# Kernel optimization log

Measured on AMD Instinct MI355X. Metric: run time of the kernel, lower is better.

The kernel has to match this reference:

```python
import jax, jax.numpy as jnp
import numpy as np

RF = 13          # receptive field with defaults
N_LAYERS = 8     # blocks(4) * layers(2)
DIMS = 32
RC = 16          # residual/dilation channels
SC = 8           # skip channels
BN_EPS = 1e-5


def conv1x1(x, W, b=None):
    # x: (B,Cin,N,T), W: (Cout,Cin)
    y = jnp.einsum('oc,bcnt->bont', W, x)
    if b is not None:
        y = y + b[None, :, None, None]
    return y


def bn_eval(x, g, b):
    # eval-mode BatchNorm2d with running_mean=0, running_var=1
    return x * (g / jnp.sqrt(1.0 + BN_EPS))[None, :, None, None] + b[None, :, None, None]


def setup_inputs() -> dict:
    key = jax.random.key(0)
    ks = jax.random.split(key, 24)
    B, N, T, days = 16, 1024, 12, 288
    inp = {}
    inp['inputs'] = jax.random.normal(ks[0], (B, 2, N, T), dtype=jnp.float32)
    inp['ind'] = jax.random.randint(ks[1], (B,), 0, days)
    # start convs (1 -> RC)
    inp['start_w'] = jax.random.normal(ks[2], (RC, 1)) * 0.05
    inp['start_b'] = jax.random.normal(ks[3], (RC,)) * 0.05
    inp['starta_w'] = jax.random.normal(ks[4], (RC, 1)) * 0.05
    inp['starta_b'] = jax.random.normal(ks[5], (RC,)) * 0.05
    # dynamic-graph node embeddings (torch.randn init)
    inp['p1'] = jax.random.normal(ks[6], (days, DIMS))
    inp['p2'] = jax.random.normal(ks[7], (N, DIMS))
    inp['p3'] = jax.random.normal(ks[8], (N, DIMS))
    inp['pk'] = jax.random.normal(ks[9], (DIMS, DIMS, DIMS))
    # shared channel-attention fcs (bias=False)
    inp['fc1_w'] = jax.random.normal(ks[10], (RC, RC)) * 0.05
    inp['fc2_w'] = jax.random.normal(ks[11], (RC, RC)) * 0.05
    # per-layer skip convs (RC -> SC)
    inp['skip_w'] = jax.random.normal(ks[12], (N_LAYERS, SC, RC)) * 0.05
    inp['skip_b'] = jax.random.normal(ks[13], (N_LAYERS, SC)) * 0.05
    # per-layer gcn mlp ((order*support_len+1)*RC = 48 -> RC)
    inp['gconv_w'] = jax.random.normal(ks[14], (N_LAYERS, RC, 3 * RC)) * 0.05
    inp['gconv_b'] = jax.random.normal(ks[15], (N_LAYERS, RC)) * 0.05
    # batchnorm affine params
    inp['bn_g'] = jnp.ones((N_LAYERS, RC)) + jax.random.normal(ks[16], (N_LAYERS, RC)) * 0.01
    inp['bn_b'] = jax.random.normal(ks[17], (N_LAYERS, RC)) * 0.01
    inp['bna_g'] = jnp.ones((N_LAYERS, RC)) + jax.random.normal(ks[18], (N_LAYERS, RC)) * 0.01
    inp['bna_b'] = jax.random.normal(ks[19], (N_LAYERS, RC)) * 0.01
    # end convs: 832 -> 64 -> 12
    inp['end1_w'] = jax.random.normal(ks[20], (64, SC * RF * N_LAYERS)) * 0.02
    inp['end1_b'] = jax.random.normal(ks[21], (64,)) * 0.02
    inp['end2_w'] = jax.random.normal(ks[22], (12, 64)) * 0.02
    inp['end2_b'] = jax.random.normal(ks[23], (12,)) * 0.02
    return inp


def reference(inputs, ind, start_w, start_b, starta_w, starta_b, p1, p2, p3, pk,
              fc1_w, fc2_w, skip_w, skip_b, gconv_w, gconv_b,
              bn_g, bn_b, bna_g, bna_b, end1_w, end1_b, end2_w, end2_b):
    B, _, N, T = inputs.shape
    if T < RF:  # static python condition
        xo = jnp.pad(inputs, ((0, 0), (0, 0), (0, 0), (RF - T, 0)))
    else:
        xo = inputs
    x = conv1x1(xo[:, 0:1], start_w, start_b)      # (B,RC,N,RF)
    x_a = conv1x1(xo[:, 1:2], starta_w, starta_b)  # (B,RC,N,RF)

    # dgconstruct: dynamic adjacency (identical for every layer -> compute once)
    te = p1[ind]                                   # (B,DIMS)
    adp = jnp.einsum('ai,ijk->ajk', te, pk)        # (B,DIMS,DIMS)
    src = jnp.einsum('bj,ajk->abk', p2, adp)       # (B,N,DIMS)
    full = jnp.einsum('ck,abk->abc', p3, src)      # (B,N,N)
    temp = full[:, :, :DIMS]                       # (B,N,DIMS)
    x1 = jnp.einsum('bnd,bmd->bnm', src, temp)     # (B,N,N)
    A = jax.nn.relu(jnp.tanh(x1 - jnp.swapaxes(x1, 1, 2)))  # x2 = x1^T

    skips = []
    for i in range(N_LAYERS):
        residual = x
        # avg-pool / max-pool to same size are identity -> avg_out == max_out
        a_out = conv1x1(jax.nn.relu(conv1x1(residual, fc1_w)), fc2_w)
        x = jax.nn.sigmoid(a_out + a_out + x)
        residual_a = x_a
        s = conv1x1(x, skip_w[i], skip_b[i])        # (B,SC,N,RF)
        skips.append(jnp.transpose(s, (0, 1, 3, 2)).reshape(B, SC * RF, N, 1))
        # gcn with support_len=1, order=2 (dropout off in eval)
        h1 = jnp.einsum('bcvl,bwv->bcwl', x, A)
        h2 = jnp.einsum('bcvl,bwv->bcwl', h1, A)
        h = jnp.concatenate([x, h1, h2], axis=1)    # (B,3*RC,N,RF)
        x = conv1x1(h, gconv_w[i], gconv_b[i])
        x = x_a + x
        x_a = x_a + residual_a
        x = x + residual
        x = bn_eval(x, bn_g[i], bn_b[i])
        x_a = bn_eval(x_a, bna_g[i], bna_b[i])

    # torch prepends each new skip: last layer's skip goes first
    skip = jnp.concatenate(skips[::-1], axis=1)     # (B,832,N,1)
    out = jax.nn.relu(skip)
    out = jax.nn.relu(conv1x1(out, end1_w, end1_b))
    out = conv1x1(out, end2_w, end2_b)              # (B,12,N,1)
    return out
```

## Files before the change

### kernel.cpp

```cpp
#include <hip/hip_runtime.h>
#include <math.h>

#define NB 16
#define NCH 16
#define NL 13
#define NN 1024
#define NT 12
#define NLAY 8
#define MROWS 208
#define MPAD 256

typedef _Float16 f16;
typedef __attribute__((ext_vector_type(8))) _Float16 f16x8;
typedef __attribute__((ext_vector_type(16))) float f32x16;

#define OFF_TAB   0
#define OFF_ADP   1024
#define OFF_M     (OFF_ADP  + (size_t)NB*1024)
#define OFF_SRC   (OFF_M    + (size_t)NB*1024)
#define OFF_TEMP  (OFF_SRC  + (size_t)NB*NN*32)
#define OFF_AH    (OFF_TEMP + (size_t)NB*NN*32)
#define OFF_XH    (OFF_AH   + (size_t)NB*NN*NN/2)
#define OFF_XL    (OFF_XH   + (size_t)NB*MPAD*NN/2)
#define OFF_H1H   (OFF_XL   + (size_t)NB*MPAD*NN/2)
#define OFF_H1L   (OFF_H1H  + (size_t)NB*MPAD*NN/2)
#define OFF_H2    (OFF_H1L  + (size_t)NB*MPAD*NN/2)
#define OFF_X     (OFF_H2   + (size_t)NB*MPAD*NN)
#define OFF_SKIP  (OFF_X    + (size_t)NB*MROWS*NN)
#define WS_FLOATS (OFF_SKIP + (size_t)NB*832*NN)

__device__ __forceinline__ void gload16(const void* g, void* l) {
    __builtin_amdgcn_global_load_lds(
        (const __attribute__((address_space(1))) unsigned int*)g,
        (__attribute__((address_space(3))) unsigned int*)l,
        16, 0, 0);
}

__device__ __forceinline__ float fast_tanh(float x) {
    float e = __expf(2.0f * x);
    return 1.0f - 2.0f / (e + 1.0f);
}

__global__ void k_tables(const float* __restrict__ bn_g,
                         const float* __restrict__ bna_g, const float* __restrict__ bna_b,
                         const float* __restrict__ sa_w, const float* __restrict__ sa_b,
                         float* __restrict__ tab) {
    int c = threadIdx.x;
    if (c >= 16) return;
    float inv = 1.0f / sqrtf(1.0f + 1e-5f);
    float A = sa_w[c], Bc = sa_b[c];
    for (int i = 0; i < NLAY; i++) {
        tab[i*16 + c]       = bn_g[i*16 + c] * inv;
        tab[128 + i*16 + c] = A;
        tab[256 + i*16 + c] = Bc;
        float ga = bna_g[i*16 + c] * inv;
        A  = 2.0f * ga * A;
        Bc = 2.0f * ga * Bc + bna_b[i*16 + c];
    }
}

__global__ __launch_bounds__(256) void k_startfc(const float* __restrict__ inp,
                        const float* __restrict__ sw, const float* __restrict__ sb,
                        const float* __restrict__ fc1, const float* __restrict__ fc2,
                        const float* __restrict__ skw, const float* __restrict__ skb,
                        float* __restrict__ x, f16* __restrict__ xh, f16* __restrict__ xl,
                        float* __restrict__ skip) {
    __shared__ float W1[256], W2[256], W3[128], B3[8], SW[16], SB[16];
    int t = threadIdx.x;
    if (t < 256) { W1[t] = fc1[t]; W2[t] = fc2[t]; }
    if (t < 128) W3[t] = skw[t];
    if (t < 8)   B3[t] = skb[t];
    if (t < 16)  { SW[t] = sw[t]; SB[t] = sb[t]; }
    __syncthreads();
    int idx = blockIdx.x*256 + t;
    int n = idx & 1023;
    int q = idx >> 10;
    int l = q % 13, b = q / 13;
    float u = (l == 0) ? 0.f : inp[((size_t)(b*2 + 0)*NN + n)*NT + (l - 1)];
    float v[16], t1[16], v2[16];
    #pragma unroll
    for (int c = 0; c < 16; c++) {
        v[c] = SW[c]*u + SB[c];
        x[((size_t)b*MROWS + c*13 + l)*NN + n] = v[c];
    }
    #pragma unroll
    for (int c = 0; c < 16; c++) {
        float s = 0.f;
        #pragma unroll
        for (int j = 0; j < 16; j++) s += W1[c*16 + j] * v[j];
        t1[c] = fmaxf(s, 0.f);
    }
    #pragma unroll
    for (int c = 0; c < 16; c++) {
        float s = 0.f;
        #pragma unroll
        for (int j = 0; j < 16; j++) s += W2[c*16 + j] * t1[j];
        float z = 2.f*s + v[c];
        v2[c] = 1.f / (1.f + __expf(-z));
        size_t o = ((size_t)b*MPAD + c*13 + l)*NN + n;
        f16 hi = (f16)v2[c];
        xh[o] = hi;
        xl[o] = (f16)(v2[c] - (float)hi);
    }
    #pragma unroll
    for (int sc = 0; sc < 8; sc++) {
        float s = B3[sc];
        #pragma unroll
        for (int c = 0; c < 16; c++) s += W3[sc*16 + c] * v2[c];
        skip[((size_t)b*832 + 7*104 + sc*13 + l)*NN + n] = s;
    }
}

__global__ __launch_bounds__(256) void k_adp(const float* __restrict__ p1, const int* __restrict__ ind,
                      const float* __restrict__ pk, const float* __restrict__ p3,
                      float* __restrict__ adpg, float* __restrict__ Mg) {
    __shared__ float te[32];
    __shared__ float adp[32][32];
    __shared__ float p3s[32][32];
    int b = blockIdx.x, t = threadIdx.x;
    if (t < 32) te[t] = p1[(size_t)ind[b]*32 + t];
    for (int i = t; i < 1024; i += 256) p3s[i >> 5][i & 31] = p3[i];
    __syncthreads();
    for (int i = t; i < 1024; i += 256) {
        float s = 0.f;
        for (int q = 0; q < 32; q++) s += te[q] * pk[q*1024 + i];
        adp[i >> 5][i & 31] = s;
        adpg[(size_t)b*1024 + i] = s;
    }
    __syncthreads();
    for (int i = t; i < 1024; i += 256) {
        int j = i >> 5, c = i & 31;
        float s = 0.f;
        for (int k = 0; k < 32; k++) s += adp[j][k] * p3s[c][k];
        Mg[(size_t)b*1024 + i] = s;
    }
}

__global__ __launch_bounds__(256) void k_st(const float* __restrict__ p2, const float* __restrict__ adpg,
                     const float* __restrict__ Mg,
                     float* __restrict__ src, float* __restrict__ temp) {
    __shared__ float adpS[32][32], MS[32][32], p2S[128][32];
    int b = blockIdx.y, n0 = blockIdx.x * 128, t = threadIdx.x;
    for (int i = t; i < 1024; i += 256) {
        adpS[i >> 5][i & 31] = adpg[(size_t)b*1024 + i];
        MS[i >> 5][i & 31]   = Mg[(size_t)b*1024 + i];
    }
    for (int i = t; i < 128*32; i += 256) p2S[i >> 5][i & 31] = p2[(size_t)(n0 + (i >> 5))*32 + (i & 31)];
    __syncthreads();
    int k = t & 31, g = t >> 5;
    for (int nn = g; nn < 128; nn += 8) {
        float rs = 0.f, rt = 0.f;
        #pragma unroll 8
        for (int j = 0; j < 32; j++) {
            float pv = p2S[nn][j];
            rs += pv * adpS[j][k];
            rt += pv * MS[j][k];
        }
        src [((size_t)b*NN + n0 + nn)*32 + k] = rs;
        temp[((size_t)b*NN + n0 + nn)*32 + k] = rt;
    }
}

__global__ __launch_bounds__(256) void k_A(const float* __restrict__ src, const float* __restrict__ temp,
                    f16* __restrict__ Amat) {
    int b = blockIdx.z;
    int r = blockIdx.x, ti = 0;
    while (r >= 16 - ti) { r -= 16 - ti; ti++; }
    int tj = ti + r;
    int n0 = ti*64, m0 = tj*64;
    __shared__ float snT[32][68], tmT[32][68], smT[32][68], tnT[32][68];
    __shared__ f16 At[64][72];
    int t = threadIdx.x;
    const float* sb_ = src  + (size_t)b*NN*32;
    const float* tb_ = temp + (size_t)b*NN*32;
    for (int i = t; i < 64*32; i += 256) {
        int rr = i >> 5, k = i & 31;
        snT[k][rr] = sb_[(n0 + rr)*32 + k];
        tmT[k][rr] = tb_[(m0 + rr)*32 + k];
        smT[k][rr] = sb_[(m0 + rr)*32 + k];
        tnT[k][rr] = tb_[(n0 + rr)*32 + k];
    }
    __syncthreads();
    int tr = (t >> 4) * 4, tc = (t & 15) * 4;
    float acc1[4][4] = {}, acc2[4][4] = {};
    #pragma unroll 4
    for (int k = 0; k < 32; k++) {
        float4 a  = *(const float4*)&snT[k][tr];
        float4 bb = *(const float4*)&tmT[k][tc];
        float4 c2 = *(const float4*)&smT[k][tc];
        float4 d2 = *(const float4*)&tnT[k][tr];
        float av[4] = {a.x, a.y, a.z, a.w};
        float bv[4] = {bb.x, bb.y, bb.z, bb.w};
        float cv[4] = {c2.x, c2.y, c2.z, c2.w};
        float dv[4] = {d2.x, d2.y, d2.z, d2.w};
        #pragma unroll
        for (int i = 0; i < 4; i++)
            #pragma unroll
            for (int jj = 0; jj < 4; jj++) { acc1[i][jj] += av[i]*bv[jj]; acc2[i][jj] += cv[jj]*dv[i]; }
    }
    #pragma unroll
    for (int i = 0; i < 4; i++)
        #pragma unroll
        for (int jj = 0; jj < 4; jj++) {
            float v = fast_tanh(acc1[i][jj] - acc2[i][jj]);
            Amat[((size_t)b*NN + n0 + tr + i)*NN + m0 + tc + jj] = (f16)(v > 0.f ? v : 0.f);
            At[tc + jj][tr + i] = (f16)(-v > 0.f ? -v : 0.f);
        }
    __syncthreads();
    for (int i = t; i < 512; i += 256) {
        int rr = i >> 3, c8 = (i & 7) * 8;
        f16* dst = &Amat[((size_t)b*NN + m0 + rr)*NN + n0 + c8];
        #pragma unroll
        for (int k = 0; k < 8; k++) dst[k] = At[rr][c8 + k];
    }
}

template<bool HOP1>
__global__ __launch_bounds__(256) void k_gmm(const f16* __restrict__ Xh, const f16* __restrict__ Xl,
                     const f16* __restrict__ Ag, float* __restrict__ Cf,
                     f16* __restrict__ Ch, f16* __restrict__ Cl) {
    __shared__ alignas(16) f16 As[2][128*64];
    __shared__ alignas(16) f16 Xs[2][2*64*64];
    const int bid = blockIdx.x;
    const int xcd = bid & 7;
    const int j   = bid >> 3;
    const int b   = xcd + ((j >> 5) << 3);
    const int tile = j & 31;
    const int my  = tile >> 3;
    const int n0  = (tile & 7) * 128;
    const int t = threadIdx.x;
    const int w = t >> 6, lane = t & 63;
    const char* Ab  = (const char*)(Ag + (size_t)b*NN*NN);
    const char* Xhb = (const char*)(Xh + (size_t)b*MPAD*NN);
    const char* Xlb = (const char*)(Xl + (size_t)b*MPAD*NN);

    const char* asrc[4];
    int adst[4];
    const char* xsrc[4];
    int xdst[4];
    {
        const char* Abase = Ab + (size_t)n0*2048;
        const char* Xb0 = Xhb + (size_t)(my*64)*2048;
        const char* Xb1 = Xlb + (size_t)(my*64)*2048;
        #pragma unroll
        for (int rr = 0; rr < 4; ++rr) {
            int q = rr*4 + w;
            int slot = q*64 + lane;
            int row = slot >> 3, ch = slot & 7;
            asrc[rr] = Abase + (size_t)row*2048 + ((ch ^ (row & 7)) << 4);
            adst[rr] = q*1024;
            int xrow = row & 63;
            xsrc[rr] = ((q >> 3) ? Xb1 : Xb0) + (size_t)xrow*2048 + ((ch ^ (xrow & 7)) << 4);
            xdst[rr] = q*1024;
        }
    }

    const int wm = (w >> 1) * 32, wn = (w & 1) * 64;
    const int kh = lane >> 5;
    const int arow = wm + (lane & 31);
    const int brow0 = wn + (lane & 31);
    const int brow1 = brow0 + 32;
    const int swa = arow & 7, swb0 = brow0 & 7, swb1 = brow1 & 7;

    f32x16 acc0 = {}, acc1 = {};

    auto stage = [&](int buf, int it) {
        size_t koff = (size_t)it * 128;
        #pragma unroll
        for (int rr = 0; rr < 4; ++rr)
            gload16(asrc[rr] + koff, (char*)As[buf] + adst[rr]);
        #pragma unroll
        for (int rr = 0; rr < 4; ++rr)
            gload16(xsrc[rr] + koff, (char*)Xs[buf] + xdst[rr]);
    };
    auto compute = [&](int buf) {
        const char* aP0 = (const char*)Xs[buf] + (size_t)arow*128;
        const char* aP1 = aP0 + 8192;
        const char* bP0 = (const char*)As[buf] + (size_t)brow0*128;
        const char* bP1 = (const char*)As[buf] + (size_t)brow1*128;
        #pragma unroll
        for (int s = 0; s < 4; ++s) {
            int cn = s*2 + kh;
            f16x8 ah = *(const f16x8*)(aP0 + ((cn ^ swa) << 4));
            f16x8 al = *(const f16x8*)(aP1 + ((cn ^ swa) << 4));
            f16x8 b0 = *(const f16x8*)(bP0 + ((cn ^ swb0) << 4));
            f16x8 b1 = *(const f16x8*)(bP1 + ((cn ^ swb1) << 4));
            acc0 = __builtin_amdgcn_mfma_f32_32x32x16_f16(ah, b0, acc0, 0, 0, 0);
            acc1 = __builtin_amdgcn_mfma_f32_32x32x16_f16(ah, b1, acc1, 0, 0, 0);
            acc0 = __builtin_amdgcn_mfma_f32_32x32x16_f16(al, b0, acc0, 0, 0, 0);
            acc1 = __builtin_amdgcn_mfma_f32_32x32x16_f16(al, b1, acc1, 0, 0, 0);
        }
    };

    stage(0, 0);
    int cur = 0;
    for (int it = 0; it < 15; ++it) {
        stage(cur ^ 1, it + 1);
        asm volatile("s_waitcnt vmcnt(8)" ::: "memory");
        __builtin_amdgcn_s_barrier();
        compute(cur);
        __builtin_amdgcn_s_barrier();
        cur ^= 1;
    }
    asm volatile("s_waitcnt vmcnt(0)" ::: "memory");
    __builtin_amdgcn_s_barrier();
    compute(cur);

    const int coll = lane & 31;
    #pragma unroll
    for (int reg = 0; reg < 16; ++reg) {
        int m = my*64 + wm + (reg & 3) + 8*(reg >> 2) + 4*kh;
        if (m < MROWS) {
            size_t o0 = ((size_t)b*MPAD + m)*NN + n0 + wn + coll;
            float v0 = acc0[reg], v1 = acc1[reg];
            if (HOP1) {
                f16 h0 = (f16)v0; Ch[o0]      = h0; Cl[o0]      = (f16)(v0 - (float)h0);
                f16 h1 = (f16)v1; Ch[o0 + 32] = h1; Cl[o0 + 32] = (f16)(v1 - (float)h1);
            } else {
                Cf[o0] = v0; Cf[o0 + 32] = v1;
            }
        }
    }
}

__global__ __launch_bounds__(256) void k_epifc(float* __restrict__ x,
                      f16* __restrict__ xh, f16* __restrict__ xl,
                      const f16* __restrict__ h1h, const f16* __restrict__ h1l,
                      const float* __restrict__ h2,
                      const float* __restrict__ inp, const float* __restrict__ gw,
                      const float* __restrict__ gb, const float* __restrict__ bnb,
                      const float* __restrict__ tab,
                      const float* __restrict__ fc1, const float* __restrict__ fc2,
                      const float* __restrict__ skw, const float* __restrict__ skb,
                      float* __restrict__ skip, int layer) {
    __shared__ float W[768], W1[256], W2[256], W3[128], B3[8];
    __shared__ float GB[16], BNBs[16], BNS[16], AC[16], BC[16];
    int t = threadIdx.x;
    for (int i = t; i < 768; i += 256) W[i] = gw[layer*768 + i];
    if (t < 256) { W1[t] = fc1[t]; W2[t] = fc2[t]; }
    int nl = layer + 1;
    if (t < 128) W3[t] = skw[nl*128 + t];
    if (t < 8)   B3[t] = skb[nl*8 + t];
    if (t < 16) {
        GB[t]   = gb[layer*16 + t];
        BNBs[t] = bnb[layer*16 + t];
        BNS[t]  = tab[layer*16 + t];
        AC[t]   = tab[128 + layer*16 + t];
        BC[t]   = tab[256 + layer*16 + t];
    }
    __syncthreads();
    int idx = blockIdx.x*256 + t;
    int n = idx & 1023;
    int q = idx >> 10;
    int l = q % 13, b = q / 13;
    float u1 = (l == 0) ? 0.f : inp[((size_t)(b*2 + 1)*NN + n)*NT + (l - 1)];
    float vx[16], v1[16], v2[16], xnew[16];
    #pragma unroll
    for (int c = 0; c < 16; c++) {
        size_t op = ((size_t)b*MPAD + c*13 + l)*NN + n;
        vx[c] = (float)xh[op] + (float)xl[op];
        v1[c] = (float)h1h[op] + (float)h1l[op];
        v2[c] = h2[op];
    }
    #pragma unroll
    for (int o = 0; o < 16; o++) {
        float s = GB[o];
        #pragma unroll
        for (int c = 0; c < 16; c++) s += W[o*48 + c]      * vx[c];
        #pragma unroll
        for (int c = 0; c < 16; c++) s += W[o*48 + 16 + c] * v1[c];
        #pragma unroll
        for (int c = 0; c < 16; c++) s += W[o*48 + 32 + c] * v2[c];
        float xa = AC[o]*u1 + BC[o];
        float vo = x[((size_t)b*MROWS + o*13 + l)*NN + n];
        xnew[o] = BNS[o]*(s + xa + vo) + BNBs[o];
    }
    if (layer < 6) {
        #pragma unroll
        for (int o = 0; o < 16; o++)
            x[((size_t)b*MROWS + o*13 + l)*NN + n] = xnew[o];
    }
    float t1[16], vs[16];
    #pragma unroll
    for (int c = 0; c < 16; c++) {
        float s = 0.f;
        #pragma unroll
        for (int j = 0; j < 16; j++) s += W1[c*16 + j] * xnew[j];
        t1[c] = fmaxf(s, 0.f);
    }
    #pragma unroll
    for (int c = 0; c < 16; c++) {
        float s = 0.f;
        #pragma unroll
        for (int j = 0; j < 16; j++) s += W2[c*16 + j] * t1[j];
        float z = 2.f*s + xnew[c];
        vs[c] = 1.f / (1.f + __expf(-z));
        if (layer < 6) {
            size_t o = ((size_t)b*MPAD + c*13 + l)*NN + n;
            f16 hi = (f16)vs[c];
            xh[o] = hi;
            xl[o] = (f16)(vs[c] - (float)hi);
        }
    }
    #pragma unroll
    for (int sc = 0; sc < 8; sc++) {
        float s = B3[sc];
        #pragma unroll
        for (int c = 0; c < 16; c++) s += W3[sc*16 + c] * vs[c];
        skip[((size_t)b*832 + (7 - nl)*104 + sc*13 + l)*NN + n] = s;
    }
}

__global__ __launch_bounds__(256) void k_end1(const float* __restrict__ skip, const float* __restrict__ w1,
                       float* __restrict__ out1) {
    __shared__ alignas(16) float Ws[52][68];
    __shared__ alignas(16) float Ss[52][68];
    int n0 = blockIdx.x * 64, ks = blockIdx.y, b = blockIdx.z;
    int t = threadIdx.x, ty = t >> 4, tx = t & 15;
    float acc[4][4] = {};
    int kbase = ks * 208;
    for (int kk = 0; kk < 4; kk++) {
        int k0 = kbase + kk*52;
        for (int i = t; i < 52*64; i += 256) {
            int r = i >> 6, c = i & 63;
            float sv = skip[((size_t)b*832 + k0 + r)*NN + n0 + c];
            Ss[r][c] = sv > 0.f ? sv : 0.f;
            Ws[r][c] = w1[(size_t)c*832 + k0 + r];
        }
        __syncthreads();
        #pragma unroll 4
        for (int k = 0; k < 52; k++) {
            float4 av = *(const float4*)&Ws[k][ty*4];
            float4 bv = *(const float4*)&Ss[k][tx*4];
            float a[4] = {av.x, av.y, av.z, av.w};
            float bb[4] = {bv.x, bv.y, bv.z, bv.w};
            #pragma unroll
            for (int i = 0; i < 4; i++)
                #pragma unroll
                for (int jj = 0; jj < 4; jj++) acc[i][jj] += a[i]*bb[jj];
        }
        __syncthreads();
    }
    #pragma unroll
    for (int i = 0; i < 4; i++)
        #pragma unroll
        for (int jj = 0; jj < 4; jj++)
            out1[(((size_t)ks*NB + b)*64 + ty*4 + i)*NN + n0 + tx*4 + jj] = acc[i][jj];
}

__global__ __launch_bounds__(256) void k_end2(const float* __restrict__ out1, const float* __restrict__ b1,
                       const float* __restrict__ w2, const float* __restrict__ b2,
                       float* __restrict__ outp) {
    __shared__ float S[64][68];
    int n0 = blockIdx.x * 64, b = blockIdx.y;
    int t = threadIdx.x;
    for (int i = t; i < 4096; i += 256) {
        int o = i >> 6, n = i & 63;
        float s = b1[o];
        #pragma unroll
        for (int ks = 0; ks < 4; ks++)
            s += out1[(((size_t)ks*NB + b)*64 + o)*NN + n0 + n];
        S[o][n] = s > 0.f ? s : 0.f;
    }
    __syncthreads();
    for (int idx = t; idx < 12*64; idx += 256) {
        int jr = idx >> 6, n = idx & 63;
        float s = b2[jr];
        for (int o = 0; o < 64; o++) s += w2[jr*64 + o] * S[o][n];
        outp[((size_t)b*12 + jr)*NN + n0 + n] = s;
    }
}

extern "C" void kernel_launch(void* const* d_in, const int* in_sizes, int n_in,
                              void* d_out, int out_size, void* d_ws, size_t ws_size,
                              hipStream_t stream) {
    (void)in_sizes; (void)n_in; (void)out_size;
    if (ws_size < WS_FLOATS * sizeof(float)) return;

    const float* inputs  = (const float*)d_in[0];
    const int*   ind     = (const int*)  d_in[1];
    const float* start_w = (const float*)d_in[2];
    const float* start_b = (const float*)d_in[3];
    const float* starta_w= (const float*)d_in[4];
    const float* starta_b= (const float*)d_in[5];
    const float* p1      = (const float*)d_in[6];
    const float* p2      = (const float*)d_in[7];
    const float* p3      = (const float*)d_in[8];
    const float* pk      = (const float*)d_in[9];
    const float* fc1_w   = (const float*)d_in[10];
    const float* fc2_w   = (const float*)d_in[11];
    const float* skip_w  = (const float*)d_in[12];
    const float* skip_b  = (const float*)d_in[13];
    const float* gconv_w = (const float*)d_in[14];
    const float* gconv_b = (const float*)d_in[15];
    const float* bn_g    = (const float*)d_in[16];
    const float* bn_b    = (const float*)d_in[17];
    const float* bna_g   = (const float*)d_in[18];
    const float* bna_b   = (const float*)d_in[19];
    const float* end1_w  = (const float*)d_in[20];
    const float* end1_b  = (const float*)d_in[21];
    const float* end2_w  = (const float*)d_in[22];
    const float* end2_b  = (const float*)d_in[23];

    float* ws   = (float*)d_ws;
    float* tab  = ws + OFF_TAB;
    float* adpg = ws + OFF_ADP;
    float* Mg   = ws + OFF_M;
    float* src  = ws + OFF_SRC;
    float* temp = ws + OFF_TEMP;
    f16*   Ah   = (f16*)(ws + OFF_AH);
    f16*   xh   = (f16*)(ws + OFF_XH);
    f16*   xl   = (f16*)(ws + OFF_XL);
    f16*   h1h  = (f16*)(ws + OFF_H1H);
    f16*   h1l  = (f16*)(ws + OFF_H1L);
    float* h2   = ws + OFF_H2;
    float* x    = ws + OFF_X;
    float* skip = ws + OFF_SKIP;

    k_tables<<<1, 64, 0, stream>>>(bn_g, bna_g, bna_b, starta_w, starta_b, tab);
    k_startfc<<<(NB*NL*NN)/256, 256, 0, stream>>>(inputs, start_w, start_b, fc1_w, fc2_w,
                                                  skip_w, skip_b, x, xh, xl, skip);
    k_adp<<<NB, 256, 0, stream>>>(p1, ind, pk, p3, adpg, Mg);
    k_st<<<dim3(8, NB), 256, 0, stream>>>(p2, adpg, Mg, src, temp);
    k_A<<<dim3(136, 1, NB), 256, 0, stream>>>(src, temp, Ah);

    for (int i = 0; i < 7; i++) {
        k_gmm<true ><<<512, 256, 0, stream>>>(xh,  xl,  Ah, nullptr, h1h, h1l);
        k_gmm<false><<<512, 256, 0, stream>>>(h1h, h1l, Ah, h2, nullptr, nullptr);
        k_epifc<<<(NB*NL*NN)/256, 256, 0, stream>>>(x, xh, xl, h1h, h1l, h2, inputs,
                                                    gconv_w, gconv_b, bn_b, tab,
                                                    fc1_w, fc2_w, skip_w, skip_b, skip, i);
    }
    k_end1<<<dim3(16, 4, NB), 256, 0, stream>>>(skip, end1_w, h2);
    k_end2<<<dim3(16, NB), 256, 0, stream>>>(h2, end1_b, end2_w, end2_b, (float*)d_out);
}
```

Baseline: 651.0 us.

## Fuse second graph-hop GEMM with gconv/attention epilogue into one kernel

Adds a kernel that computes the second adjacency multiplication for a 64-column tile of one batch across all channel rows. It keeps the fp32 result in LDS and runs the gconv, batchnorm, channel-attention and skip epilogue directly on it. This drops the fp32 h2 round trip through global memory and one kernel launch per layer. In exchange the GEMM runs with 256 larger blocks instead of 512, and the serial epilogue loop now follows the MFMA phase inside each block.

```diff
diff --git a/kernel.cpp b/kernel.cpp
--- a/kernel.cpp
+++ b/kernel.cpp
@@ -215,10 +215,8 @@
     }
 }
 
-template<bool HOP1>
 __global__ __launch_bounds__(256) void k_gmm(const f16* __restrict__ Xh, const f16* __restrict__ Xl,
-                     const f16* __restrict__ Ag, float* __restrict__ Cf,
-                     f16* __restrict__ Ch, f16* __restrict__ Cl) {
+                     const f16* __restrict__ Ag, f16* __restrict__ Ch, f16* __restrict__ Cl) {
     __shared__ alignas(16) f16 As[2][128*64];
     __shared__ alignas(16) f16 Xs[2][2*64*64];
     const int bid = blockIdx.x;
@@ -313,101 +311,185 @@
         if (m < MROWS) {
             size_t o0 = ((size_t)b*MPAD + m)*NN + n0 + wn + coll;
             float v0 = acc0[reg], v1 = acc1[reg];
-            if (HOP1) {
-                f16 h0 = (f16)v0; Ch[o0]      = h0; Cl[o0]      = (f16)(v0 - (float)h0);
-                f16 h1 = (f16)v1; Ch[o0 + 32] = h1; Cl[o0 + 32] = (f16)(v1 - (float)h1);
-            } else {
-                Cf[o0] = v0; Cf[o0 + 32] = v1;
+            f16 h0 = (f16)v0; Ch[o0]      = h0; Cl[o0]      = (f16)(v0 - (float)h0);
+            f16 h1 = (f16)v1; Ch[o0 + 32] = h1; Cl[o0 + 32] = (f16)(v1 - (float)h1);
+        }
+    }
+}
+
+__global__ __launch_bounds__(256) void k_g2e(
+        const f16* __restrict__ h1h, const f16* __restrict__ h1l,
+        const f16* __restrict__ Ag,
+        f16* __restrict__ xh, f16* __restrict__ xl,
+        float* __restrict__ x, const float* __restrict__ inp,
+        const float* __restrict__ gw, const float* __restrict__ gb,
+        const float* __restrict__ bnb, const float* __restrict__ tab,
+        const float* __restrict__ fc1, const float* __restrict__ fc2,
+        const float* __restrict__ skw, const float* __restrict__ skb,
+        float* __restrict__ skip, int layer) {
+    __shared__ alignas(16) char lds[2*36864];
+    __shared__ float Wg[768], W1s[256], W2s[256], W3s[128], B3s[8];
+    __shared__ float GBs[16], BNBs[16], BNSs[16], ACs[16], BCs[16];
+    const int bid = blockIdx.x;
+    const int xcd = bid & 7, g = bid >> 3;
+    const int b   = xcd + ((g & 1) << 3);
+    const int n0  = (g >> 1) * 64;
+    const int t = threadIdx.x, w = t >> 6, lane = t & 63;
+    const int nl = layer + 1;
+
+    const char* sp[9];
+    {
+        const char* H0 = (const char*)(h1h + (size_t)b*MPAD*NN);
+        const char* H1 = (const char*)(h1l + (size_t)b*MPAD*NN);
+        const char* Ab = (const char*)(Ag  + (size_t)b*NN*NN);
+        #pragma unroll
+        for (int i = 0; i < 8; ++i) {
+            int s16 = (i & 3)*256 + t;
+            int row = s16 >> 2, ch = s16 & 3;
+            sp[i] = ((i < 4) ? H0 : H1) + (size_t)row*2048 + ((ch ^ (row & 3)) << 4);
+        }
+        int row = t >> 2, ch = t & 3;
+        sp[8] = Ab + (size_t)(n0 + row)*2048 + ((ch ^ (row & 3)) << 4);
+    }
+
+    f32x16 acc00 = {}, acc01 = {}, acc10 = {}, acc11 = {};
+    const int r0 = w*64 + (lane & 31);
+    const int kh = lane >> 5;
+    const int c0 = lane & 31;
+    const int swA = r0 & 3, swB0 = c0 & 3;
+
+    auto stage = [&](int buf, int it) {
+        size_t koff = (size_t)it * 64;
+        char* dbase = lds + buf*36864 + w*1024;
+        #pragma unroll
+        for (int i = 0; i < 9; ++i)
+            gload16(sp[i] + koff, dbase + i*4096);
+    };
+    auto compute = [&](int buf) {
+        const char* H = lds + buf*36864;
+        const char* Areg = H + 32768;
+        #pragma unroll
+        for (int s = 0; s < 2; ++s) {
+            int cn = s*2 + kh;
+            const char* a0p = H + r0*64 + ((cn ^ swA) << 4);
+            const char* a1p = a0p + 32*64;
+            f16x8 a0h = *(const f16x8*)(a0p);
+            f16x8 a0l = *(const f16x8*)(a0p + 16384);
+            f16x8 a1h = *(const f16x8*)(a1p);
+            f16x8 a1l = *(const f16x8*)(a1p + 16384);
+            const char* b0p = Areg + c0*64 + ((cn ^ swB0) << 4);
+            const char* b1p = b0p + 32*64;
+            f16x8 bb0 = *(const f16x8*)b0p;
+            f16x8 bb1 = *(const f16x8*)b1p;
+            acc00 = __builtin_amdgcn_mfma_f32_32x32x16_f16(a0h, bb0, acc00, 0, 0, 0);
+            acc01 = __builtin_amdgcn_mfma_f32_32x32x16_f16(a0h, bb1, acc01, 0, 0, 0);
+            acc10 = __builtin_amdgcn_mfma_f32_32x32x16_f16(a1h, bb0, acc10, 0, 0, 0);
+            acc11 = __builtin_amdgcn_mfma_f32_32x32x16_f16(a1h, bb1, acc11, 0, 0, 0);
+            acc00 = __builtin_amdgcn_mfma_f32_32x32x16_f16(a0l, bb0, acc00, 0, 0, 0);
+            acc01 = __builtin_amdgcn_mfma_f32_32x32x16_f16(a0l, bb1, acc01, 0, 0, 0);
+            acc10 = __builtin_amdgcn_mfma_f32_32x32x16_f16(a1l, bb0, acc10, 0, 0, 0);
+            acc11 = __builtin_amdgcn_mfma_f32_32x32x16_f16(a1l, bb1, acc11, 0, 0, 0);
+        }
+    };
+
+    stage(0, 0);
+    for (int i = t; i < 768; i += 256) Wg[i] = gw[layer*768 + i];
+    if (t < 256) { W1s[t] = fc1[t]; W2s[t] = fc2[t]; }
+    if (t < 128) W3s[t] = skw[nl*128 + t];
+    if (t < 8)   B3s[t] = skb[nl*8 + t];
+    if (t < 16) {
+        GBs[t]  = gb[layer*16 + t];
+        BNBs[t] = bnb[layer*16 + t];
+        BNSs[t] = tab[layer*16 + t];
+        ACs[t]  = tab[128 + layer*16 + t];
+        BCs[t]  = tab[256 + layer*16 + t];
+    }
+
+    int cur = 0;
+    for (int it = 0; it < 31; ++it) {
+        stage(cur ^ 1, it + 1);
+        asm volatile("s_waitcnt vmcnt(9)" ::: "memory");
+        __builtin_amdgcn_s_barrier();
+        compute(cur);
+        __builtin_amdgcn_s_barrier();
+        cur ^= 1;
+    }
+    asm volatile("s_waitcnt vmcnt(0)" ::: "memory");
+    __builtin_amdgcn_s_barrier();
+    compute(cur);
+    __builtin_amdgcn_s_barrier();
+
+    float* H2 = (float*)lds;
+    #pragma unroll
+    for (int reg = 0; reg < 16; ++reg) {
+        int mrow = (reg & 3) + 8*(reg >> 2) + 4*kh;
+        H2[(w*64 + mrow)*64      + c0     ] = acc00[reg];
+        H2[(w*64 + mrow)*64      + c0 + 32] = acc01[reg];
+        H2[(w*64 + 32 + mrow)*64 + c0     ] = acc10[reg];
+        H2[(w*64 + 32 + mrow)*64 + c0 + 32] = acc11[reg];
+    }
+    __syncthreads();
+
+    for (int pos = t; pos < 13*64; pos += 256) {
+        int l = pos >> 6, n = pos & 63;
+        int gn = n0 + n;
+        float u1 = (l == 0) ? 0.f : inp[((size_t)(b*2 + 1)*NN + gn)*NT + (l - 1)];
+        float vx[16], v1[16], v2[16], xnew[16];
+        #pragma unroll
+        for (int c = 0; c < 16; c++) {
+            int m = c*13 + l;
+            size_t op = ((size_t)b*MPAD + m)*NN + gn;
+            vx[c] = (float)xh[op] + (float)xl[op];
+            v1[c] = (float)h1h[op] + (float)h1l[op];
+            v2[c] = H2[m*64 + n];
+        }
+        #pragma unroll
+        for (int o = 0; o < 16; o++) {
+            float s = GBs[o];
+            #pragma unroll
+            for (int c = 0; c < 16; c++) s += Wg[o*48 + c]      * vx[c];
+            #pragma unroll
+            for (int c = 0; c < 16; c++) s += Wg[o*48 + 16 + c] * v1[c];
+            #pragma unroll
+            for (int c = 0; c < 16; c++) s += Wg[o*48 + 32 + c] * v2[c];
+            float xa = ACs[o]*u1 + BCs[o];
+            float vo = x[((size_t)b*MROWS + o*13 + l)*NN + gn];
+            xnew[o] = BNSs[o]*(s + xa + vo) + BNBs[o];
+        }
+        if (layer < 6) {
+            #pragma unroll
+            for (int o = 0; o < 16; o++)
+                x[((size_t)b*MROWS + o*13 + l)*NN + gn] = xnew[o];
+        }
+        float t1[16], vs[16];
+        #pragma unroll
+        for (int c = 0; c < 16; c++) {
+            float s = 0.f;
+            #pragma unroll
+            for (int j = 0; j < 16; j++) s += W1s[c*16 + j] * xnew[j];
+            t1[c] = fmaxf(s, 0.f);
+        }
+        #pragma unroll
+        for (int c = 0; c < 16; c++) {
+            float s = 0.f;
+            #pragma unroll
+            for (int j = 0; j < 16; j++) s += W2s[c*16 + j] * t1[j];
+            float z = 2.f*s + xnew[c];
+            vs[c] = 1.f / (1.f + __expf(-z));
+            if (layer < 6) {
+                size_t o = ((size_t)b*MPAD + c*13 + l)*NN + gn;
+                f16 hi = (f16)vs[c];
+                xh[o] = hi;
+                xl[o] = (f16)(vs[c] - (float)hi);
             }
         }
-    }
-}
-
-__global__ __launch_bounds__(256) void k_epifc(float* __restrict__ x,
-                      f16* __restrict__ xh, f16* __restrict__ xl,
-                      const f16* __restrict__ h1h, const f16* __restrict__ h1l,
-                      const float* __restrict__ h2,
-                      const float* __restrict__ inp, const float* __restrict__ gw,
-                      const float* __restrict__ gb, const float* __restrict__ bnb,
-                      const float* __restrict__ tab,
-                      const float* __restrict__ fc1, const float* __restrict__ fc2,
-                      const float* __restrict__ skw, const float* __restrict__ skb,
-                      float* __restrict__ skip, int layer) {
-    __shared__ float W[768], W1[256], W2[256], W3[128], B3[8];
-    __shared__ float GB[16], BNBs[16], BNS[16], AC[16], BC[16];
-    int t = threadIdx.x;
-    for (int i = t; i < 768; i += 256) W[i] = gw[layer*768 + i];
-    if (t < 256) { W1[t] = fc1[t]; W2[t] = fc2[t]; }
-    int nl = layer + 1;
-    if (t < 128) W3[t] = skw[nl*128 + t];
-    if (t < 8)   B3[t] = skb[nl*8 + t];
-    if (t < 16) {
-        GB[t]   = gb[layer*16 + t];
-        BNBs[t] = bnb[layer*16 + t];
-        BNS[t]  = tab[layer*16 + t];
-        AC[t]   = tab[128 + layer*16 + t];
-        BC[t]   = tab[256 + layer*16 + t];
-    }
-    __syncthreads();
-    int idx = blockIdx.x*256 + t;
-    int n = idx & 1023;
-    int q = idx >> 10;
-    int l = q % 13, b = q / 13;
-    float u1 = (l == 0) ? 0.f : inp[((size_t)(b*2 + 1)*NN + n)*NT + (l - 1)];
-    float vx[16], v1[16], v2[16], xnew[16];
-    #pragma unroll
-    for (int c = 0; c < 16; c++) {
-        size_t op = ((size_t)b*MPAD + c*13 + l)*NN + n;
-        vx[c] = (float)xh[op] + (float)xl[op];
-        v1[c] = (float)h1h[op] + (float)h1l[op];
-        v2[c] = h2[op];
-    }
-    #pragma unroll
-    for (int o = 0; o < 16; o++) {
-        float s = GB[o];
-        #pragma unroll
-        for (int c = 0; c < 16; c++) s += W[o*48 + c]      * vx[c];
-        #pragma unroll
-        for (int c = 0; c < 16; c++) s += W[o*48 + 16 + c] * v1[c];
-        #pragma unroll
-        for (int c = 0; c < 16; c++) s += W[o*48 + 32 + c] * v2[c];
-        float xa = AC[o]*u1 + BC[o];
-        float vo = x[((size_t)b*MROWS + o*13 + l)*NN + n];
-        xnew[o] = BNS[o]*(s + xa + vo) + BNBs[o];
-    }
-    if (layer < 6) {
-        #pragma unroll
-        for (int o = 0; o < 16; o++)
-            x[((size_t)b*MROWS + o*13 + l)*NN + n] = xnew[o];
-    }
-    float t1[16], vs[16];
-    #pragma unroll
-    for (int c = 0; c < 16; c++) {
-        float s = 0.f;
-        #pragma unroll
-        for (int j = 0; j < 16; j++) s += W1[c*16 + j] * xnew[j];
-        t1[c] = fmaxf(s, 0.f);
-    }
-    #pragma unroll
-    for (int c = 0; c < 16; c++) {
-        float s = 0.f;
-        #pragma unroll
-        for (int j = 0; j < 16; j++) s += W2[c*16 + j] * t1[j];
-        float z = 2.f*s + xnew[c];
-        vs[c] = 1.f / (1.f + __expf(-z));
-        if (layer < 6) {
-            size_t o = ((size_t)b*MPAD + c*13 + l)*NN + n;
-            f16 hi = (f16)vs[c];
-            xh[o] = hi;
-            xl[o] = (f16)(vs[c] - (float)hi);
-        }
-    }
-    #pragma unroll
-    for (int sc = 0; sc < 8; sc++) {
-        float s = B3[sc];
-        #pragma unroll
-        for (int c = 0; c < 16; c++) s += W3[sc*16 + c] * vs[c];
-        skip[((size_t)b*832 + (7 - nl)*104 + sc*13 + l)*NN + n] = s;
+        #pragma unroll
+        for (int sc = 0; sc < 8; sc++) {
+            float s = B3s[sc];
+            #pragma unroll
+            for (int c = 0; c < 16; c++) s += W3s[sc*16 + c] * vs[c];
+            skip[((size_t)b*832 + (7 - nl)*104 + sc*13 + l)*NN + gn] = s;
+        }
     }
 }
 
@@ -513,7 +595,7 @@
     f16*   xl   = (f16*)(ws + OFF_XL);
     f16*   h1h  = (f16*)(ws + OFF_H1H);
     f16*   h1l  = (f16*)(ws + OFF_H1L);
-    float* h2   = ws + OFF_H2;
+    float* out1 = ws + OFF_H2;
     float* x    = ws + OFF_X;
     float* skip = ws + OFF_SKIP;
 
@@ -525,12 +607,11 @@
     k_A<<<dim3(136, 1, NB), 256, 0, stream>>>(src, temp, Ah);
 
     for (int i = 0; i < 7; i++) {
-        k_gmm<true ><<<512, 256, 0, stream>>>(xh,  xl,  Ah, nullptr, h1h, h1l);
-        k_gmm<false><<<512, 256, 0, stream>>>(h1h, h1l, Ah, h2, nullptr, nullptr);
-        k_epifc<<<(NB*NL*NN)/256, 256, 0, stream>>>(x, xh, xl, h1h, h1l, h2, inputs,
-                                                    gconv_w, gconv_b, bn_b, tab,
-                                                    fc1_w, fc2_w, skip_w, skip_b, skip, i);
-    }
-    k_end1<<<dim3(16, 4, NB), 256, 0, stream>>>(skip, end1_w, h2);
-    k_end2<<<dim3(16, NB), 256, 0, stream>>>(h2, end1_b, end2_w, end2_b, (float*)d_out);
-}
+        k_gmm<<<512, 256, 0, stream>>>(xh, xl, Ah, h1h, h1l);
+        k_g2e<<<256, 256, 0, stream>>>(h1h, h1l, Ah, xh, xl, x, inputs,
+                                       gconv_w, gconv_b, bn_b, tab,
+                                       fc1_w, fc2_w, skip_w, skip_b, skip, i);
+    }
+    k_end1<<<dim3(16, 4, NB), 256, 0, stream>>>(skip, end1_w, out1);
+    k_end2<<<dim3(16, NB), 256, 0, stream>>>(out1, end1_b, end2_w, end2_b, (float*)d_out);
+}
```

Measured after the change: 1.042 ms. +60.1%, slower.
